# Performance work log

Hardware: AMD Instinct MI355X
Metric: run time of the kernel (lower is better)

## Reference

```python
import jax, jax.numpy as jnp
import numpy as np
import math
from jax import lax

WINDOWS = (3, 5, 7)
GRIDSIZE = 3
HALF_H = 384  # hidden of each directional LSTM (d_model // 2)


def _lstm_last(x, mask, Wih, Whh, bih, bhh, reverse):
    """Masked single-layer LSTM; returns final hidden state.
    x: [N, T, D], mask: [N, T] bool. Invalid steps leave (h, c) unchanged,
    which is equivalent to running the LSTM only over the valid contiguous
    sub-window (leading/trailing pads are skipped).
    PyTorch gate order: i, f, g, o.
    """
    N = x.shape[0]
    H = Whh.shape[1]
    h0 = jnp.zeros((N, H), x.dtype)
    c0 = jnp.zeros((N, H), x.dtype)

    def step(carry, inp):
        h, c = carry
        xt, mt = inp
        gates = xt @ Wih.T + h @ Whh.T + (bih + bhh)
        i, f, g, o = jnp.split(gates, 4, axis=-1)
        i = jax.nn.sigmoid(i); f = jax.nn.sigmoid(f); o = jax.nn.sigmoid(o)
        g = jnp.tanh(g)
        c_new = f * c + i * g
        h_new = o * jnp.tanh(c_new)
        m = mt[:, None]
        return (jnp.where(m, h_new, h), jnp.where(m, c_new, c)), None

    xs = (jnp.moveaxis(x, 1, 0), jnp.moveaxis(mask, 1, 0))
    (h, _), _ = lax.scan(step, (h0, c0), xs, reverse=reverse)
    return h


def setup_inputs() -> dict:
    key = jax.random.key(0)
    ks = jax.random.split(key, 12)
    B, L, D = 16, 512, 768
    H4 = 4 * HALF_H
    s = 0.02
    inp = {
        'sequence_output': jax.random.normal(ks[0], (B, L, D), jnp.float32),
        'Wih_f': jax.random.normal(ks[1], (3, H4, D), jnp.float32) * s,
        'Whh_f': jax.random.normal(ks[2], (3, H4, HALF_H), jnp.float32) * s,
        'bih_f': jax.random.normal(ks[3], (3, H4), jnp.float32) * s,
        'bhh_f': jax.random.normal(ks[4], (3, H4), jnp.float32) * s,
        'Wih_b': jax.random.normal(ks[5], (3, H4, D), jnp.float32) * s,
        'Whh_b': jax.random.normal(ks[6], (3, H4, HALF_H), jnp.float32) * s,
        'bih_b': jax.random.normal(ks[7], (3, H4), jnp.float32) * s,
        'bhh_b': jax.random.normal(ks[8], (3, H4), jnp.float32) * s,
        'kan_coeffs': jax.random.normal(ks[9], (2, 11, GRIDSIZE, D), jnp.float32)
                      / (np.sqrt(D) * np.sqrt(GRIDSIZE)),
        'kan_bias': jax.random.normal(ks[10], (11,), jnp.float32) * s,
        'valid_ids': jax.random.randint(ks[11], (B, L), 0, 2, jnp.int64),
    }
    return inp


def reference(sequence_output, Wih_f, Whh_f, bih_f, bhh_f,
              Wih_b, Whh_b, bih_b, bhh_b, kan_coeffs, kan_bias, valid_ids):
    B, L, D = sequence_output.shape
    # ---- valid-id compaction (scatter valid tokens to the front, zeros after)
    v = valid_ids == 1
    dest = jnp.where(v, jnp.cumsum(v, axis=1) - 1, L)  # invalid -> dump slot L
    bidx = jnp.arange(B)[:, None]
    valid_output = (jnp.zeros((B, L + 1, D), sequence_output.dtype)
                    .at[bidx, dest].set(sequence_output))[:, :L]
    x = valid_output  # dropout is identity in eval

    # ---- per-window sliding BiLSTM (vectorized over all B*L positions)
    outs = []
    for wi, w in enumerate(WINDOWS):
        half = w // 2
        idx = jnp.arange(L)[:, None] + jnp.arange(-half, half + 1)[None, :]  # [L,w]
        valid = (idx >= 0) & (idx < L)
        idxc = jnp.clip(idx, 0, L - 1)
        xw = x[:, idxc].reshape(B * L, w, D)                  # [B*L, w, D]
        m = jnp.broadcast_to(valid[None], (B, L, w)).reshape(B * L, w)
        hf = _lstm_last(xw, m, Wih_f[wi], Whh_f[wi], bih_f[wi], bhh_f[wi], False)
        hb = _lstm_last(xw, m, Wih_b[wi], Whh_b[wi], bih_b[wi], bhh_b[wi], True)
        outs.append(jnp.concatenate([hf, hb], axis=-1).reshape(B, L, D))

    seq = outs[0] + outs[1] + outs[2]

    # ---- 'dot-att' fusion over window features
    stk = jnp.stack(outs, axis=2)                             # [B, L, K, D]
    q = seq[:, :, None, :]                                    # [B, L, 1, D]
    attn = jax.nn.softmax(
        jnp.einsum('blqd,blkd->blqk', q, stk) / math.sqrt(D), axis=-1)
    local = jnp.einsum('blqk,blkd->blqd', attn, stk)[:, :, 0]
    seq = seq + local

    # ---- NaiveFourierKAN classifier (gridsize=3)
    k = jnp.arange(1, GRIDSIZE + 1, dtype=seq.dtype)
    xg = seq[..., None, :] * k[:, None]                       # [B, L, g, D]
    logits = (jnp.einsum('blgi,ogi->blo', jnp.cos(xg), kan_coeffs[0])
              + jnp.einsum('blgi,ogi->blo', jnp.sin(xg), kan_coeffs[1])
              + kan_bias)
    return logits
```

## Files before the change

kernel.cpp:

```cpp
#include <hip/hip_runtime.h>

#define BT 8192
#define SEQL 512
#define DIM 768
#define HID 384
#define NG 1536

using US = unsigned short;
typedef __bf16 bf16x8 __attribute__((ext_vector_type(8)));
typedef float f32x4 __attribute__((ext_vector_type(4)));

__device__ __forceinline__ float b2f(US u) {
  union { unsigned u; float f; } x; x.u = ((unsigned)u) << 16; return x.f;
}
__device__ __forceinline__ US f2b(float f) {
  __bf16 h = (__bf16)f;
  union { __bf16 h; US u; } x; x.h = h; return x.u;
}
__device__ __forceinline__ float fsig(float x) { return 1.f / (1.f + __expf(-x)); }
__device__ __forceinline__ float ftanh(float x) { return 1.f - 2.f / (__expf(2.f * x) + 1.f); }

__device__ __forceinline__ void gload16(const void* g, void* l) {
  __builtin_amdgcn_global_load_lds((const __attribute__((address_space(1))) unsigned*)g,
                                   (__attribute__((address_space(3))) unsigned*)l, 16, 0, 0);
}

__device__ __forceinline__ bf16x8 lds_frag(const US* base, int row, int colb, int swz) {
  return *(const bf16x8*)((const char*)base + row * 128 + (colb ^ swz));
}

__global__ __launch_bounds__(256) void convW_ih_k(const float* __restrict__ WihF,
                                                  const float* __restrict__ WihB,
                                                  US* __restrict__ WihP) {
  int d = blockIdx.z;
  const float* src = d ? WihB : WihF;
  size_t idx = (size_t)blockIdx.x * 256 + threadIdx.x;
  int lane = (int)(idx & 63);
  int t = (int)(idx >> 6);
  int sg = t & 3;
  int wn = (t >> 2) & 1;
  int kk = (t >> 3) & 1;
  int kt = (t >> 4) % 12;
  int nb = (t / 192) % 12;
  int wi = t / (192 * 12);
  int srow = sg * HID + nb * 32 + wn * 16 + (lane & 15);
  int scol = kt * 64 + kk * 32 + (lane >> 4) * 8;
  const float* s = src + ((size_t)wi * NG + srow) * DIM + scol;
  float4 v0 = *(const float4*)s;
  float4 v1 = *(const float4*)(s + 4);
  ushort4 o0, o1;
  o0.x = f2b(v0.x); o0.y = f2b(v0.y); o0.z = f2b(v0.z); o0.w = f2b(v0.w);
  o1.x = f2b(v1.x); o1.y = f2b(v1.y); o1.z = f2b(v1.z); o1.w = f2b(v1.w);
  US* dst = WihP + ((size_t)d * 442368 + idx) * 8;
  *(ushort4*)dst = o0;
  *(ushort4*)(dst + 4) = o1;
}

__global__ __launch_bounds__(256) void convW_hh_k(const float* __restrict__ WhhF,
                                                  const float* __restrict__ WhhB,
                                                  US* __restrict__ WhhP) {
  int d = blockIdx.z;
  const float* src = d ? WhhB : WhhF;
  size_t idx = (size_t)blockIdx.x * 256 + threadIdx.x;
  int lane = (int)(idx & 63);
  int t = (int)(idx >> 6);
  int sg = t & 3;
  int wn = (t >> 2) & 1;
  int kk = (t >> 3) & 1;
  int kt = (t >> 4) % 6;
  int hb = (t / 96) % 12;
  int wi = t / (96 * 12);
  int srow = sg * HID + hb * 32 + wn * 16 + (lane & 15);
  int scol = kt * 64 + kk * 32 + (lane >> 4) * 8;
  const float* s = src + ((size_t)wi * NG + srow) * HID + scol;
  float4 v0 = *(const float4*)s;
  float4 v1 = *(const float4*)(s + 4);
  ushort4 o0, o1;
  o0.x = f2b(v0.x); o0.y = f2b(v0.y); o0.z = f2b(v0.z); o0.w = f2b(v0.w);
  o1.x = f2b(v1.x); o1.y = f2b(v1.y); o1.z = f2b(v1.z); o1.w = f2b(v1.w);
  US* dst = WhhP + ((size_t)d * 221184 + idx) * 8;
  *(ushort4*)dst = o0;
  *(ushort4*)(dst + 4) = o1;
}

__global__ __launch_bounds__(256) void conv_coef_k(const float* __restrict__ coef,
                                                   US* __restrict__ coefP) {
  int idx = blockIdx.x * 256 + threadIdx.x;
  int s = idx & 31;
  int i = (idx >> 5) % DIM;
  int g = idx / (32 * DIM);
  float v = 0.f;
  int o = s & 15;
  if (o < 11) v = coef[(size_t)((s >> 4) * 33 + o * 3 + g) * DIM + i];
  coefP[idx] = f2b(v);
}

__global__ void scan_k(const int* __restrict__ valid, int* __restrict__ dest) {
  __shared__ int s[SEQL];
  int b = blockIdx.x, l = threadIdx.x;
  int v = (valid[b * SEQL + l] == 1) ? 1 : 0;
  s[l] = v;
  __syncthreads();
  for (int off = 1; off < SEQL; off <<= 1) {
    int t = (l >= off) ? s[l - off] : 0;
    __syncthreads();
    s[l] += t;
    __syncthreads();
  }
  dest[b * SEQL + l] = v ? (s[l] - 1) : -1;
}

__global__ __launch_bounds__(256) void scatter_k(const float* __restrict__ seq,
                                                 const int* __restrict__ dest,
                                                 US* __restrict__ xc) {
  int idx = blockIdx.x * 256 + threadIdx.x;
  int p = idx / 192, c = idx - p * 192;
  int d = dest[p];
  if (d < 0) return;
  int b = p >> 9;
  float4 v = ((const float4*)seq)[(size_t)p * 192 + c];
  ushort4 o;
  o.x = f2b(v.x); o.y = f2b(v.y); o.z = f2b(v.z); o.w = f2b(v.w);
  ((ushort4*)xc)[(size_t)(b * SEQL + d) * 192 + c] = o;
}

__global__ __launch_bounds__(256, 4) void gate_gemm_k(
    const US* __restrict__ xc, const US* __restrict__ WihP,
    const float* __restrict__ bihF, const float* __restrict__ bihB,
    const float* __restrict__ bhhF, const float* __restrict__ bhhB,
    US* __restrict__ G, int dirBase) {
  int zi = blockIdx.z;
  int wi = zi % 3, dr = dirBase + zi / 3;
  const float* bih = dr ? bihB : bihF;
  const float* bhh = dr ? bhhB : bhhF;
  int m0 = blockIdx.x * 128, nb = blockIdx.y;
  const US* Wp = WihP + ((size_t)(dr * 3 + wi) * 12 + nb) * (128 * DIM);
  US* Gw = G + (size_t)wi * BT * NG;
  __shared__ alignas(16) US As[2][128 * 64];
  __shared__ float biasS[128];
  int tid = threadIdx.x, lane = tid & 63, wid = tid >> 6;
  int wm = wid >> 1, wn = wid & 1;
  if (tid < 128) {
    int sg = tid >> 5, hl = tid & 31;
    int gc = wi * NG + sg * HID + nb * 32 + hl;
    biasS[tid] = bih[gc] + bhh[gc];
  }
  int r_in = lane >> 3;
  int cb = (lane & 7) * 16;
  int cb_src = cb ^ (r_in << 4);
  int swz = (lane & 7) << 4;
  f32x4 acc[4][4] = {};

  auto stageA = [&](US* dst, int k0) {
#pragma unroll
    for (int c = 0; c < 4; ++c) {
      int chk = wid * 4 + c;
      int row = chk * 8 + r_in;
      gload16((const char*)xc + ((size_t)(m0 + row) * DIM + k0) * 2 + cb_src,
              (char*)dst + chk * 1024);
    }
  };

  const US* Bbase = Wp + (size_t)wn * 4 * 512 + (size_t)lane * 8;

  stageA(As[0], 0);
  __syncthreads();
  int cur = 0;
  for (int kt = 0; kt < 12; ++kt) {
    int k0 = kt * 64;
    if (k0 + 64 < DIM) stageA(As[cur ^ 1], k0 + 64);
#pragma unroll
    for (int kk = 0; kk < 2; ++kk) {
      int colb = kk * 64 + (lane >> 4) * 16;
      bf16x8 a[4], b[4];
#pragma unroll
      for (int i = 0; i < 4; ++i)
        a[i] = lds_frag(As[cur], wm * 64 + i * 16 + (lane & 15), colb, swz);
      const US* bp = Bbase + (size_t)(kt * 2 + kk) * (2 * 4 * 512);
#pragma unroll
      for (int sg = 0; sg < 4; ++sg)
        b[sg] = *(const bf16x8*)(bp + (size_t)sg * 512);
#pragma unroll
      for (int mi = 0; mi < 4; ++mi)
#pragma unroll
        for (int sg = 0; sg < 4; ++sg)
          acc[mi][sg] = __builtin_amdgcn_mfma_f32_16x16x32_bf16(a[mi], b[sg], acc[mi][sg], 0, 0, 0);
    }
    __syncthreads();
    cur ^= 1;
  }
  int hh = wn * 16 + (lane & 15);
  int hidx = nb * 32 + hh;
#pragma unroll
  for (int mi = 0; mi < 4; ++mi) {
#pragma unroll
    for (int r = 0; r < 4; ++r) {
      int p = m0 + wm * 64 + mi * 16 + ((lane >> 4) << 2) + r;
      ushort4 gv;
      gv.x = f2b(acc[mi][0][r] + biasS[hh]);
      gv.y = f2b(acc[mi][1][r] + biasS[32 + hh]);
      gv.z = f2b(acc[mi][2][r] + biasS[64 + hh]);
      gv.w = f2b(acc[mi][3][r] + biasS[96 + hh]);
      *(ushort4*)&Gw[(size_t)p * NG + (size_t)hidx * 4] = gv;
    }
  }
}

__global__ __launch_bounds__(384) void step0_k(const US* __restrict__ G, US* __restrict__ C,
                                               US* __restrict__ hn, int dirBase) {
  int zi = blockIdx.z;
  int wi = zi % 3, dr = dirBase + zi / 3;
  int half = wi + 1;
  int dlt = dr ? half : -half;
  int p = blockIdx.x, hidx = threadIdx.x;
  int l = p & (SEQL - 1);
  const US* Gw = G + (size_t)wi * BT * NG;
  float c = 0.f, h = 0.f;
  int t = l + dlt;
  if ((unsigned)t < (unsigned)SEQL) {
    ushort4 gv = *(const ushort4*)&Gw[(size_t)(p + dlt) * NG + (size_t)hidx * 4];
    c = fsig(b2f(gv.x)) * ftanh(b2f(gv.z));
    h = fsig(b2f(gv.w)) * ftanh(c);
  }
  size_t o = (size_t)wi * BT * HID + (size_t)p * HID + hidx;
  C[o] = f2b(c);
  hn[o] = f2b(h);
}

__global__ __launch_bounds__(256, 4) void step_k(
    const US* __restrict__ WhhP,
    const US* __restrict__ G, US* __restrict__ C,
    const US* __restrict__ hcur, US* __restrict__ hnxt, US* __restrict__ Outs,
    int s, int wi0, int nact, int dirBase) {
  int zi = blockIdx.z;
  int wi = wi0 + zi % nact, dr = dirBase + zi / nact;
  int w = 2 * wi + 3, half = wi + 1;
  int j = dr ? (w - 1 - s) : s;
  int dlt = j - half;
  bool fin = (s == w - 1);
  const US* Gw = G + (size_t)wi * BT * NG;
  US* Cw = C + (size_t)wi * BT * HID;
  const US* hc = hcur + (size_t)wi * BT * HID;
  US* hn = hnxt + (size_t)wi * BT * HID;
  US* Ow = Outs + (size_t)wi * BT * DIM + (dr ? HID : 0);
  int m0 = blockIdx.x * 128, hb = blockIdx.y;
  const US* Wp = WhhP + ((size_t)(dr * 3 + wi) * 12 + hb) * (128 * HID);
  __shared__ alignas(16) US As[2][128 * 64];
  int tid = threadIdx.x, lane = tid & 63, wid = tid >> 6;
  int wm = wid >> 1, wn = wid & 1;
  int r_in = lane >> 3, cb = (lane & 7) * 16;
  int cb_src = cb ^ (r_in << 4);
  int swz = (lane & 7) << 4;
  f32x4 acc[4][4] = {};

  auto stageA = [&](US* dst, int k0) {
#pragma unroll
    for (int c = 0; c < 4; ++c) {
      int chk = wid * 4 + c;
      int row = chk * 8 + r_in;
      gload16((const char*)hc + ((size_t)(m0 + row) * HID + k0) * 2 + cb_src,
              (char*)dst + chk * 1024);
    }
  };

  const US* Bbase = Wp + (size_t)wn * 4 * 512 + (size_t)lane * 8;

  stageA(As[0], 0);
  __syncthreads();
  int cur = 0;
  for (int kt = 0; kt < 6; ++kt) {
    int k0 = kt * 64;
    if (k0 + 64 < HID) stageA(As[cur ^ 1], k0 + 64);
#pragma unroll
    for (int kk = 0; kk < 2; ++kk) {
      int colb = kk * 64 + (lane >> 4) * 16;
      bf16x8 a[4], b[4];
#pragma unroll
      for (int i = 0; i < 4; ++i)
        a[i] = lds_frag(As[cur], wm * 64 + i * 16 + (lane & 15), colb, swz);
      const US* bp = Bbase + (size_t)(kt * 2 + kk) * (2 * 4 * 512);
#pragma unroll
      for (int sg = 0; sg < 4; ++sg)
        b[sg] = *(const bf16x8*)(bp + (size_t)sg * 512);
#pragma unroll
      for (int mi = 0; mi < 4; ++mi)
#pragma unroll
        for (int sg = 0; sg < 4; ++sg)
          acc[mi][sg] = __builtin_amdgcn_mfma_f32_16x16x32_bf16(a[mi], b[sg], acc[mi][sg], 0, 0, 0);
    }
    __syncthreads();
    cur ^= 1;
  }
  int hh = wn * 16 + (lane & 15);
  int hidx = hb * 32 + hh;
#pragma unroll
  for (int mi = 0; mi < 4; ++mi) {
#pragma unroll
    for (int r = 0; r < 4; ++r) {
      int p = m0 + wm * 64 + mi * 16 + ((lane >> 4) << 2) + r;
      int l = p & (SEQL - 1);
      float hval;
      if ((unsigned)(l + dlt) < (unsigned)SEQL) {
        ushort4 gv = *(const ushort4*)&Gw[(size_t)(p + dlt) * NG + (size_t)hidx * 4];
        float gi = acc[mi][0][r] + b2f(gv.x);
        float gf = acc[mi][1][r] + b2f(gv.y);
        float gg = acc[mi][2][r] + b2f(gv.z);
        float go = acc[mi][3][r] + b2f(gv.w);
        size_t ci = (size_t)p * HID + hidx;
        float c = fsig(gf) * b2f(Cw[ci]) + fsig(gi) * ftanh(gg);
        Cw[ci] = f2b(c);
        hval = fsig(go) * ftanh(c);
      } else {
        hval = b2f(hc[(size_t)p * HID + hidx]);
      }
      if (fin) Ow[(size_t)p * DIM + hidx] = f2b(hval);
      else hn[(size_t)p * HID + hidx] = f2b(hval);
    }
  }
}

__global__ __launch_bounds__(256) void attn_kan_k(
    const US* __restrict__ Outs, const US* __restrict__ coefP,
    const float* __restrict__ kbias, float* __restrict__ out) {
  int p4 = blockIdx.x * 4;
  int tid = threadIdx.x, lane = tid & 63, wid = tid >> 6;
  __shared__ float red[176];
  float sq[3][4];
  {
    float o0[3][4], o1[3][4], o2[3][4], q[3][4];
#pragma unroll
    for (int c = 0; c < 3; ++c) {
      int i = tid + 256 * c;
#pragma unroll
      for (int t = 0; t < 4; ++t) {
        o0[c][t] = b2f(Outs[(size_t)(p4 + t) * DIM + i]);
        o1[c][t] = b2f(Outs[(size_t)(BT + p4 + t) * DIM + i]);
        o2[c][t] = b2f(Outs[(size_t)(2 * BT + p4 + t) * DIM + i]);
        q[c][t] = o0[c][t] + o1[c][t] + o2[c][t];
      }
    }
    float d[3][4];
#pragma unroll
    for (int t = 0; t < 4; ++t) {
      d[0][t] = 0.f; d[1][t] = 0.f; d[2][t] = 0.f;
#pragma unroll
      for (int c = 0; c < 3; ++c) {
        d[0][t] += q[c][t] * o0[c][t];
        d[1][t] += q[c][t] * o1[c][t];
        d[2][t] += q[c][t] * o2[c][t];
      }
    }
#pragma unroll
    for (int off = 32; off; off >>= 1)
#pragma unroll
      for (int t = 0; t < 4; ++t) {
        d[0][t] += __shfl_down(d[0][t], off);
        d[1][t] += __shfl_down(d[1][t], off);
        d[2][t] += __shfl_down(d[2][t], off);
      }
    if (lane == 0)
#pragma unroll
      for (int t = 0; t < 4; ++t) {
        red[(t * 3 + 0) * 4 + wid] = d[0][t];
        red[(t * 3 + 1) * 4 + wid] = d[1][t];
        red[(t * 3 + 2) * 4 + wid] = d[2][t];
      }
    __syncthreads();
    const float scl = 0.03608439182435161f;
#pragma unroll
    for (int t = 0; t < 4; ++t) {
      float s0 = (red[(t * 3) * 4] + red[(t * 3) * 4 + 1] + red[(t * 3) * 4 + 2] + red[(t * 3) * 4 + 3]) * scl;
      float s1 = (red[(t * 3 + 1) * 4] + red[(t * 3 + 1) * 4 + 1] + red[(t * 3 + 1) * 4 + 2] + red[(t * 3 + 1) * 4 + 3]) * scl;
      float s2 = (red[(t * 3 + 2) * 4] + red[(t * 3 + 2) * 4 + 1] + red[(t * 3 + 2) * 4 + 2] + red[(t * 3 + 2) * 4 + 3]) * scl;
      float mx = fmaxf(s0, fmaxf(s1, s2));
      float a0 = __expf(s0 - mx), a1 = __expf(s1 - mx), a2 = __expf(s2 - mx);
      float inv = 1.f / (a0 + a1 + a2);
      a0 *= inv; a1 *= inv; a2 *= inv;
#pragma unroll
      for (int c = 0; c < 3; ++c)
        sq[c][t] = q[c][t] + a0 * o0[c][t] + a1 * o1[c][t] + a2 * o2[c][t];
    }
  }
  float acc[11][4];
#pragma unroll
  for (int o = 0; o < 11; ++o)
#pragma unroll
    for (int t = 0; t < 4; ++t) acc[o][t] = 0.f;
#pragma unroll
  for (int c = 0; c < 3; ++c) {
    int i = tid + 256 * c;
#pragma unroll
    for (int g = 0; g < 3; ++g) {
      float sn[4], cs[4];
#pragma unroll
      for (int t = 0; t < 4; ++t) __sincosf(sq[c][t] * (float)(g + 1), &sn[t], &cs[t]);
      const US* cp = coefP + ((size_t)g * DIM + i) * 32;
      bf16x8 k0 = *(const bf16x8*)(cp);
      bf16x8 k1 = *(const bf16x8*)(cp + 8);
      bf16x8 k2 = *(const bf16x8*)(cp + 16);
      bf16x8 k3 = *(const bf16x8*)(cp + 24);
#pragma unroll
      for (int o = 0; o < 8; ++o) {
        float cc = (float)k0[o], ss = (float)k2[o];
#pragma unroll
        for (int t = 0; t < 4; ++t) acc[o][t] += cs[t] * cc + sn[t] * ss;
      }
#pragma unroll
      for (int o = 8; o < 11; ++o) {
        float cc = (float)k1[o - 8], ss = (float)k3[o - 8];
#pragma unroll
        for (int t = 0; t < 4; ++t) acc[o][t] += cs[t] * cc + sn[t] * ss;
      }
    }
  }
  __syncthreads();
#pragma unroll
  for (int o = 0; o < 11; ++o)
#pragma unroll
    for (int t = 0; t < 4; ++t) {
      float v = acc[o][t];
#pragma unroll
      for (int off = 32; off; off >>= 1) v += __shfl_down(v, off);
      if (lane == 0) red[(o * 4 + t) * 4 + wid] = v;
    }
  __syncthreads();
  if (tid < 44) {
    int o = tid >> 2, t = tid & 3;
    out[(size_t)(p4 + t) * 11 + o] =
        red[tid * 4] + red[tid * 4 + 1] + red[tid * 4 + 2] + red[tid * 4 + 3] + kbias[o];
  }
}

extern "C" void kernel_launch(void* const* d_in, const int* in_sizes, int n_in,
                              void* d_out, int out_size, void* d_ws, size_t ws_size,
                              hipStream_t stream) {
  const float* seq = (const float*)d_in[0];
  const float* WihF = (const float*)d_in[1];
  const float* WhhF = (const float*)d_in[2];
  const float* bihF = (const float*)d_in[3];
  const float* bhhF = (const float*)d_in[4];
  const float* WihB = (const float*)d_in[5];
  const float* WhhB = (const float*)d_in[6];
  const float* bihB = (const float*)d_in[7];
  const float* bhhB = (const float*)d_in[8];
  const float* coef = (const float*)d_in[9];
  const float* kbias = (const float*)d_in[10];
  const int* valid = (const int*)d_in[11];

  constexpr size_t SZ_XC = (size_t)BT * DIM * 2;
  constexpr size_t SZ_DEST = (size_t)BT * 4;
  constexpr size_t SZ_CP = (size_t)3 * DIM * 32 * 2;
  constexpr size_t SZ_G = (size_t)3 * BT * NG * 2;
  constexpr size_t SZ_C = (size_t)3 * BT * HID * 2;
  constexpr size_t SZ_H = (size_t)3 * BT * HID * 2;
  constexpr size_t SZ_OUTS = (size_t)3 * BT * DIM * 2;
  constexpr size_t SZ_WIHP = (size_t)2 * 3 * NG * DIM * 2;
  constexpr size_t SZ_WHHP = (size_t)2 * 3 * NG * HID * 2;
  constexpr size_t NEED = SZ_XC + SZ_DEST + SZ_CP + SZ_WIHP + SZ_WHHP +
                          SZ_G + SZ_C + 2 * SZ_H + SZ_OUTS;
  if (ws_size < NEED) return;

  char* ws = (char*)d_ws;
  US* xc = (US*)ws;                          ws += SZ_XC;
  int* dest = (int*)ws;                      ws += SZ_DEST;
  US* coefP = (US*)ws;                       ws += SZ_CP;
  US* WihP = (US*)ws;                        ws += SZ_WIHP;
  US* WhhP = (US*)ws;                        ws += SZ_WHHP;
  US* G = (US*)ws;                           ws += SZ_G;
  US* C = (US*)ws;                           ws += SZ_C;
  US* h0 = (US*)ws;                          ws += SZ_H;
  US* h1 = (US*)ws;                          ws += SZ_H;
  US* Outs = (US*)ws;
  float* out = (float*)d_out;

  hipMemsetAsync(xc, 0, SZ_XC, stream);
  scan_k<<<16, SEQL, 0, stream>>>(valid, dest);
  scatter_k<<<(BT * 192) / 256, 256, 0, stream>>>(seq, dest, xc);
  conv_coef_k<<<288, 256, 0, stream>>>(coef, coefP);
  convW_ih_k<<<dim3(442368 / 256, 1, 2), 256, 0, stream>>>(WihF, WihB, WihP);
  convW_hh_k<<<dim3(221184 / 256, 1, 2), 256, 0, stream>>>(WhhF, WhhB, WhhP);

  for (int dir = 0; dir < 2; ++dir) {
    gate_gemm_k<<<dim3(64, 12, 3), 256, 0, stream>>>(xc, WihP, bihF, bihB, bhhF, bhhB, G, dir);
    step0_k<<<dim3(BT, 1, 3), HID, 0, stream>>>(G, C, h1, dir);
    for (int s = 1; s < 7; ++s) {
      int nact = (s < 3) ? 3 : ((s < 5) ? 2 : 1);
      int wi0 = 3 - nact;
      US* hcur = (s & 1) ? h1 : h0;
      US* hnxt = (s & 1) ? h0 : h1;
      step_k<<<dim3(64, 12, nact), 256, 0, stream>>>(WhhP, G, C, hcur, hnxt, Outs,
                                                     s, wi0, nact, dir);
    }
  }
  attn_kan_k<<<BT / 4, 256, 0, stream>>>(Outs, coefP, kbias, out);
}
```

Baseline: 794.8 us.

## Fuse all LSTM recurrence steps into one persistent kernel with LDS-resident state

Replaces the per-timestep step0_k/step_k launches with a single kernel per direction. Each block owns 32 rows of one window and loops over all timesteps, keeping h and c in shared memory and never writing them to global memory. This removes about 14 launches and the global round trips of h and c. In exchange each block reloads the full Whh slice from global or L2 on every step, works on a small 32-row M tile with lower MFMA reuse, and has far fewer blocks per launch (768), so per-step weight bandwidth may become the bottleneck.

Measured after the change: 1.240 ms. 56.0% more time.

```diff
diff --git a/kernel.cpp b/kernel.cpp
--- a/kernel.cpp
+++ b/kernel.cpp
@@ -5,6 +5,7 @@
 #define DIM 768
 #define HID 384
 #define NG 1536
+#define FM 32
 
 using US = unsigned short;
 typedef __bf16 bf16x8 __attribute__((ext_vector_type(8)));
@@ -206,116 +207,88 @@
   }
 }
 
-__global__ __launch_bounds__(384) void step0_k(const US* __restrict__ G, US* __restrict__ C,
-                                               US* __restrict__ hn, int dirBase) {
-  int zi = blockIdx.z;
-  int wi = zi % 3, dr = dirBase + zi / 3;
-  int half = wi + 1;
-  int dlt = dr ? half : -half;
-  int p = blockIdx.x, hidx = threadIdx.x;
-  int l = p & (SEQL - 1);
+__global__ __launch_bounds__(256) void lstm_fused_k(
+    const US* __restrict__ WhhP, const US* __restrict__ G,
+    US* __restrict__ Outs, int dir) {
+  int x = blockIdx.x;
+  int wi = x % 3;
+  int m0 = (x / 3) * FM;
+  int w = 2 * wi + 3, half = wi + 1;
   const US* Gw = G + (size_t)wi * BT * NG;
-  float c = 0.f, h = 0.f;
-  int t = l + dlt;
-  if ((unsigned)t < (unsigned)SEQL) {
-    ushort4 gv = *(const ushort4*)&Gw[(size_t)(p + dlt) * NG + (size_t)hidx * 4];
-    c = fsig(b2f(gv.x)) * ftanh(b2f(gv.z));
-    h = fsig(b2f(gv.w)) * ftanh(c);
-  }
-  size_t o = (size_t)wi * BT * HID + (size_t)p * HID + hidx;
-  C[o] = f2b(c);
-  hn[o] = f2b(h);
-}
-
-__global__ __launch_bounds__(256, 4) void step_k(
-    const US* __restrict__ WhhP,
-    const US* __restrict__ G, US* __restrict__ C,
-    const US* __restrict__ hcur, US* __restrict__ hnxt, US* __restrict__ Outs,
-    int s, int wi0, int nact, int dirBase) {
-  int zi = blockIdx.z;
-  int wi = wi0 + zi % nact, dr = dirBase + zi / nact;
-  int w = 2 * wi + 3, half = wi + 1;
-  int j = dr ? (w - 1 - s) : s;
-  int dlt = j - half;
-  bool fin = (s == w - 1);
-  const US* Gw = G + (size_t)wi * BT * NG;
-  US* Cw = C + (size_t)wi * BT * HID;
-  const US* hc = hcur + (size_t)wi * BT * HID;
-  US* hn = hnxt + (size_t)wi * BT * HID;
-  US* Ow = Outs + (size_t)wi * BT * DIM + (dr ? HID : 0);
-  int m0 = blockIdx.x * 128, hb = blockIdx.y;
-  const US* Wp = WhhP + ((size_t)(dr * 3 + wi) * 12 + hb) * (128 * HID);
-  __shared__ alignas(16) US As[2][128 * 64];
-  int tid = threadIdx.x, lane = tid & 63, wid = tid >> 6;
-  int wm = wid >> 1, wn = wid & 1;
-  int r_in = lane >> 3, cb = (lane & 7) * 16;
-  int cb_src = cb ^ (r_in << 4);
-  int swz = (lane & 7) << 4;
-  f32x4 acc[4][4] = {};
-
-  auto stageA = [&](US* dst, int k0) {
-#pragma unroll
-    for (int c = 0; c < 4; ++c) {
-      int chk = wid * 4 + c;
-      int row = chk * 8 + r_in;
-      gload16((const char*)hc + ((size_t)(m0 + row) * HID + k0) * 2 + cb_src,
-              (char*)dst + chk * 1024);
-    }
-  };
-
-  const US* Bbase = Wp + (size_t)wn * 4 * 512 + (size_t)lane * 8;
-
-  stageA(As[0], 0);
-  __syncthreads();
-  int cur = 0;
-  for (int kt = 0; kt < 6; ++kt) {
-    int k0 = kt * 64;
-    if (k0 + 64 < HID) stageA(As[cur ^ 1], k0 + 64);
-#pragma unroll
-    for (int kk = 0; kk < 2; ++kk) {
-      int colb = kk * 64 + (lane >> 4) * 16;
-      bf16x8 a[4], b[4];
-#pragma unroll
-      for (int i = 0; i < 4; ++i)
-        a[i] = lds_frag(As[cur], wm * 64 + i * 16 + (lane & 15), colb, swz);
-      const US* bp = Bbase + (size_t)(kt * 2 + kk) * (2 * 4 * 512);
-#pragma unroll
-      for (int sg = 0; sg < 4; ++sg)
-        b[sg] = *(const bf16x8*)(bp + (size_t)sg * 512);
-#pragma unroll
-      for (int mi = 0; mi < 4; ++mi)
-#pragma unroll
-        for (int sg = 0; sg < 4; ++sg)
-          acc[mi][sg] = __builtin_amdgcn_mfma_f32_16x16x32_bf16(a[mi], b[sg], acc[mi][sg], 0, 0, 0);
+  US* Ow = Outs + (size_t)wi * BT * DIM + (dir ? HID : 0);
+  const US* WpB = WhhP + (size_t)(dir * 3 + wi) * 12 * (128 * HID);
+
+  __shared__ alignas(16) US h_lds[2][FM * HID];
+  __shared__ alignas(16) US c_lds[FM * HID];
+
+  int tid = threadIdx.x, lane = tid & 63, wv = tid >> 6;
+  int l15 = lane & 15, l4 = lane >> 4;
+
+  for (int s = 0; s < w; ++s) {
+    int j = dir ? (w - 1 - s) : s;
+    int dlt = j - half;
+    bool fin = (s == w - 1);
+    const US* hprev = h_lds[(s + 1) & 1];
+    US* hnext = h_lds[s & 1];
+
+#pragma unroll 1
+    for (int ch = 0; ch < 6; ++ch) {
+      int hbase = wv * 96 + ch * 16;
+      int hidx = hbase + l15;
+      f32x4 acc[2][4] = {};
+      if (s > 0) {
+        int hb = hbase >> 5, wn = (hbase >> 4) & 1;
+        const US* Bb = WpB + (size_t)hb * (128 * HID) + (size_t)wn * 2048 + (size_t)lane * 8;
+#pragma unroll
+        for (int kk = 0; kk < 12; ++kk) {
+          int colb = kk * 64 + l4 * 16;
+          bf16x8 a[2], b[4];
+#pragma unroll
+          for (int mi = 0; mi < 2; ++mi) {
+            int rr = mi * 16 + l15;
+            a[mi] = *(const bf16x8*)((const char*)hprev + rr * (HID * 2) +
+                                     (colb ^ ((rr & 7) << 4)));
+          }
+          const US* bp = Bb + (size_t)kk * 4096;
+#pragma unroll
+          for (int sg = 0; sg < 4; ++sg)
+            b[sg] = *(const bf16x8*)(bp + (size_t)sg * 512);
+#pragma unroll
+          for (int mi = 0; mi < 2; ++mi)
+#pragma unroll
+            for (int sg = 0; sg < 4; ++sg)
+              acc[mi][sg] = __builtin_amdgcn_mfma_f32_16x16x32_bf16(a[mi], b[sg], acc[mi][sg], 0, 0, 0);
+        }
+      }
+#pragma unroll
+      for (int mi = 0; mi < 2; ++mi) {
+#pragma unroll
+        for (int r = 0; r < 4; ++r) {
+          int rloc = mi * 16 + (l4 << 2) + r;
+          int p = m0 + rloc;
+          int l = p & (SEQL - 1);
+          int sb = rloc * (HID * 2) + ((hidx * 2) ^ ((rloc & 7) << 4));
+          float hval;
+          if ((unsigned)(l + dlt) < (unsigned)SEQL) {
+            ushort4 gv = *(const ushort4*)&Gw[(size_t)(p + dlt) * NG + (size_t)hidx * 4];
+            float gi = acc[mi][0][r] + b2f(gv.x);
+            float gf = acc[mi][1][r] + b2f(gv.y);
+            float gg = acc[mi][2][r] + b2f(gv.z);
+            float go = acc[mi][3][r] + b2f(gv.w);
+            float cold = (s == 0) ? 0.f : b2f(*(const US*)((const char*)c_lds + sb));
+            float c = fsig(gf) * cold + fsig(gi) * ftanh(gg);
+            *(US*)((char*)c_lds + sb) = f2b(c);
+            hval = fsig(go) * ftanh(c);
+          } else {
+            hval = (s == 0) ? 0.f : b2f(*(const US*)((const char*)hprev + sb));
+            if (s == 0) *(US*)((char*)c_lds + sb) = 0;
+          }
+          if (fin) Ow[(size_t)p * DIM + hidx] = f2b(hval);
+          else *(US*)((char*)hnext + sb) = f2b(hval);
+        }
+      }
     }
     __syncthreads();
-    cur ^= 1;
-  }
-  int hh = wn * 16 + (lane & 15);
-  int hidx = hb * 32 + hh;
-#pragma unroll
-  for (int mi = 0; mi < 4; ++mi) {
-#pragma unroll
-    for (int r = 0; r < 4; ++r) {
-      int p = m0 + wm * 64 + mi * 16 + ((lane >> 4) << 2) + r;
-      int l = p & (SEQL - 1);
-      float hval;
-      if ((unsigned)(l + dlt) < (unsigned)SEQL) {
-        ushort4 gv = *(const ushort4*)&Gw[(size_t)(p + dlt) * NG + (size_t)hidx * 4];
-        float gi = acc[mi][0][r] + b2f(gv.x);
-        float gf = acc[mi][1][r] + b2f(gv.y);
-        float gg = acc[mi][2][r] + b2f(gv.z);
-        float go = acc[mi][3][r] + b2f(gv.w);
-        size_t ci = (size_t)p * HID + hidx;
-        float c = fsig(gf) * b2f(Cw[ci]) + fsig(gi) * ftanh(gg);
-        Cw[ci] = f2b(c);
-        hval = fsig(go) * ftanh(c);
-      } else {
-        hval = b2f(hc[(size_t)p * HID + hidx]);
-      }
-      if (fin) Ow[(size_t)p * DIM + hidx] = f2b(hval);
-      else hn[(size_t)p * HID + hidx] = f2b(hval);
-    }
   }
 }
 
@@ -451,13 +424,11 @@
   constexpr size_t SZ_DEST = (size_t)BT * 4;
   constexpr size_t SZ_CP = (size_t)3 * DIM * 32 * 2;
   constexpr size_t SZ_G = (size_t)3 * BT * NG * 2;
-  constexpr size_t SZ_C = (size_t)3 * BT * HID * 2;
-  constexpr size_t SZ_H = (size_t)3 * BT * HID * 2;
   constexpr size_t SZ_OUTS = (size_t)3 * BT * DIM * 2;
   constexpr size_t SZ_WIHP = (size_t)2 * 3 * NG * DIM * 2;
   constexpr size_t SZ_WHHP = (size_t)2 * 3 * NG * HID * 2;
   constexpr size_t NEED = SZ_XC + SZ_DEST + SZ_CP + SZ_WIHP + SZ_WHHP +
-                          SZ_G + SZ_C + 2 * SZ_H + SZ_OUTS;
+                          SZ_G + SZ_OUTS;
   if (ws_size < NEED) return;
 
   char* ws = (char*)d_ws;
@@ -467,9 +438,6 @@
   US* WihP = (US*)ws;                        ws += SZ_WIHP;
   US* WhhP = (US*)ws;                        ws += SZ_WHHP;
   US* G = (US*)ws;                           ws += SZ_G;
-  US* C = (US*)ws;                           ws += SZ_C;
-  US* h0 = (US*)ws;                          ws += SZ_H;
-  US* h1 = (US*)ws;                          ws += SZ_H;
   US* Outs = (US*)ws;
   float* out = (float*)d_out;
 
@@ -482,15 +450,7 @@
 
   for (int dir = 0; dir < 2; ++dir) {
     gate_gemm_k<<<dim3(64, 12, 3), 256, 0, stream>>>(xc, WihP, bihF, bihB, bhhF, bhhB, G, dir);
-    step0_k<<<dim3(BT, 1, 3), HID, 0, stream>>>(G, C, h1, dir);
-    for (int s = 1; s < 7; ++s) {
-      int nact = (s < 3) ? 3 : ((s < 5) ? 2 : 1);
-      int wi0 = 3 - nact;
-      US* hcur = (s & 1) ? h1 : h0;
-      US* hnxt = (s & 1) ? h0 : h1;
-      step_k<<<dim3(64, 12, nact), 256, 0, stream>>>(WhhP, G, C, hcur, hnxt, Outs,
-                                                     s, wi0, nact, dir);
-    }
+    lstm_fused_k<<<(BT / FM) * 3, 256, 0, stream>>>(WhhP, G, Outs, dir);
   }
   attn_kan_k<<<BT / 4, 256, 0, stream>>>(Outs, coefP, kbias, out);
 }
```

## Pre-pack activations into MFMA fragment layout and drop LDS staging in GEMMs

Applied to the files above, without the earlier changes.

The compacted input xc and the hidden-state buffers are now written directly in a fragment-packed panel layout (pk_off), matching the layout already used for the weights. The gate GEMM and recurrent step GEMM then load A fragments straight from global memory with coalesced 16-byte loads, removing the global_load_lds staging, LDS swizzle reads, double buffering and the per-iteration barriers. This trades LDS reuse and software pipelining for simpler direct loads that depend on L1/L2 caching. Scatter, step0 and the step epilogue write hidden state in the packed layout.

Result: no change. 805.6 us (+1.4%).

```diff
diff --git a/kernel.cpp b/kernel.cpp
--- a/kernel.cpp
+++ b/kernel.cpp
@@ -20,13 +20,10 @@
 __device__ __forceinline__ float fsig(float x) { return 1.f / (1.f + __expf(-x)); }
 __device__ __forceinline__ float ftanh(float x) { return 1.f - 2.f / (__expf(2.f * x) + 1.f); }
 
-__device__ __forceinline__ void gload16(const void* g, void* l) {
-  __builtin_amdgcn_global_load_lds((const __attribute__((address_space(1))) unsigned*)g,
-                                   (__attribute__((address_space(3))) unsigned*)l, 16, 0, 0);
-}
-
-__device__ __forceinline__ bf16x8 lds_frag(const US* base, int row, int colb, int swz) {
-  return *(const bf16x8*)((const char*)base + row * 128 + (colb ^ swz));
+__device__ __forceinline__ size_t pk_off(int panel, int rloc, int col, int panelStride) {
+  return (size_t)panel * panelStride + (col >> 6) * 8192 + ((col >> 5) & 1) * 4096 +
+         (rloc >> 6) * 2048 + ((rloc >> 4) & 3) * 512 +
+         (((rloc & 15) | (((col & 31) >> 3) << 4))) * 8 + (col & 7);
 }
 
 __global__ __launch_bounds__(256) void convW_ih_k(const float* __restrict__ WihF,
@@ -112,20 +109,23 @@
 
 __global__ __launch_bounds__(256) void scatter_k(const float* __restrict__ seq,
                                                  const int* __restrict__ dest,
-                                                 US* __restrict__ xc) {
+                                                 US* __restrict__ xcP) {
   int idx = blockIdx.x * 256 + threadIdx.x;
-  int p = idx / 192, c = idx - p * 192;
+  int p = idx / 192, cc = idx - p * 192;
   int d = dest[p];
   if (d < 0) return;
   int b = p >> 9;
-  float4 v = ((const float4*)seq)[(size_t)p * 192 + c];
+  float4 v = ((const float4*)seq)[(size_t)p * 192 + cc];
   ushort4 o;
   o.x = f2b(v.x); o.y = f2b(v.y); o.z = f2b(v.z); o.w = f2b(v.w);
-  ((ushort4*)xc)[(size_t)(b * SEQL + d) * 192 + c] = o;
+  int pdst = b * SEQL + d;
+  int c = cc * 4;
+  size_t off = pk_off(pdst >> 7, pdst & 127, c, 98304);
+  *(ushort4*)&xcP[off] = o;
 }
 
 __global__ __launch_bounds__(256, 4) void gate_gemm_k(
-    const US* __restrict__ xc, const US* __restrict__ WihP,
+    const US* __restrict__ xcP, const US* __restrict__ WihP,
     const float* __restrict__ bihF, const float* __restrict__ bihB,
     const float* __restrict__ bhhF, const float* __restrict__ bhhB,
     US* __restrict__ G, int dirBase) {
@@ -133,10 +133,9 @@
   int wi = zi % 3, dr = dirBase + zi / 3;
   const float* bih = dr ? bihB : bihF;
   const float* bhh = dr ? bhhB : bhhF;
-  int m0 = blockIdx.x * 128, nb = blockIdx.y;
-  const US* Wp = WihP + ((size_t)(dr * 3 + wi) * 12 + nb) * (128 * DIM);
+  int panel = blockIdx.x, nb = blockIdx.y;
+  const US* Wp = WihP + ((size_t)(dr * 3 + wi) * 12 + nb) * 98304;
   US* Gw = G + (size_t)wi * BT * NG;
-  __shared__ alignas(16) US As[2][128 * 64];
   __shared__ float biasS[128];
   int tid = threadIdx.x, lane = tid & 63, wid = tid >> 6;
   int wm = wid >> 1, wn = wid & 1;
@@ -145,52 +144,28 @@
     int gc = wi * NG + sg * HID + nb * 32 + hl;
     biasS[tid] = bih[gc] + bhh[gc];
   }
-  int r_in = lane >> 3;
-  int cb = (lane & 7) * 16;
-  int cb_src = cb ^ (r_in << 4);
-  int swz = (lane & 7) << 4;
+  __syncthreads();
   f32x4 acc[4][4] = {};
-
-  auto stageA = [&](US* dst, int k0) {
-#pragma unroll
-    for (int c = 0; c < 4; ++c) {
-      int chk = wid * 4 + c;
-      int row = chk * 8 + r_in;
-      gload16((const char*)xc + ((size_t)(m0 + row) * DIM + k0) * 2 + cb_src,
-              (char*)dst + chk * 1024);
-    }
-  };
-
-  const US* Bbase = Wp + (size_t)wn * 4 * 512 + (size_t)lane * 8;
-
-  stageA(As[0], 0);
-  __syncthreads();
-  int cur = 0;
-  for (int kt = 0; kt < 12; ++kt) {
-    int k0 = kt * 64;
-    if (k0 + 64 < DIM) stageA(As[cur ^ 1], k0 + 64);
-#pragma unroll
-    for (int kk = 0; kk < 2; ++kk) {
-      int colb = kk * 64 + (lane >> 4) * 16;
-      bf16x8 a[4], b[4];
-#pragma unroll
-      for (int i = 0; i < 4; ++i)
-        a[i] = lds_frag(As[cur], wm * 64 + i * 16 + (lane & 15), colb, swz);
-      const US* bp = Bbase + (size_t)(kt * 2 + kk) * (2 * 4 * 512);
+  const US* Ab = xcP + (size_t)panel * 98304 + (size_t)wm * 2048 + (size_t)lane * 8;
+  const US* Bb = Wp + (size_t)wn * 2048 + (size_t)lane * 8;
+#pragma unroll 2
+  for (int kp = 0; kp < 24; ++kp) {
+    bf16x8 a[4], b[4];
+    const US* ap = Ab + (size_t)kp * 4096;
+    const US* bp = Bb + (size_t)kp * 4096;
+#pragma unroll
+    for (int mi = 0; mi < 4; ++mi) a[mi] = *(const bf16x8*)(ap + (size_t)mi * 512);
+#pragma unroll
+    for (int sg = 0; sg < 4; ++sg) b[sg] = *(const bf16x8*)(bp + (size_t)sg * 512);
+#pragma unroll
+    for (int mi = 0; mi < 4; ++mi)
 #pragma unroll
       for (int sg = 0; sg < 4; ++sg)
-        b[sg] = *(const bf16x8*)(bp + (size_t)sg * 512);
-#pragma unroll
-      for (int mi = 0; mi < 4; ++mi)
-#pragma unroll
-        for (int sg = 0; sg < 4; ++sg)
-          acc[mi][sg] = __builtin_amdgcn_mfma_f32_16x16x32_bf16(a[mi], b[sg], acc[mi][sg], 0, 0, 0);
-    }
-    __syncthreads();
-    cur ^= 1;
+        acc[mi][sg] = __builtin_amdgcn_mfma_f32_16x16x32_bf16(a[mi], b[sg], acc[mi][sg], 0, 0, 0);
   }
   int hh = wn * 16 + (lane & 15);
   int hidx = nb * 32 + hh;
+  int m0 = panel * 128;
 #pragma unroll
   for (int mi = 0; mi < 4; ++mi) {
 #pragma unroll
@@ -222,9 +197,8 @@
     c = fsig(b2f(gv.x)) * ftanh(b2f(gv.z));
     h = fsig(b2f(gv.w)) * ftanh(c);
   }
-  size_t o = (size_t)wi * BT * HID + (size_t)p * HID + hidx;
-  C[o] = f2b(c);
-  hn[o] = f2b(h);
+  C[(size_t)wi * BT * HID + (size_t)p * HID + hidx] = f2b(c);
+  hn[(size_t)wi * BT * HID + pk_off(p >> 7, p & 127, hidx, 49152)] = f2b(h);
 }
 
 __global__ __launch_bounds__(256, 4) void step_k(
@@ -243,62 +217,42 @@
   const US* hc = hcur + (size_t)wi * BT * HID;
   US* hn = hnxt + (size_t)wi * BT * HID;
   US* Ow = Outs + (size_t)wi * BT * DIM + (dr ? HID : 0);
-  int m0 = blockIdx.x * 128, hb = blockIdx.y;
-  const US* Wp = WhhP + ((size_t)(dr * 3 + wi) * 12 + hb) * (128 * HID);
-  __shared__ alignas(16) US As[2][128 * 64];
+  int panel = blockIdx.x, hb = blockIdx.y;
+  const US* Wp = WhhP + ((size_t)(dr * 3 + wi) * 12 + hb) * 49152;
   int tid = threadIdx.x, lane = tid & 63, wid = tid >> 6;
   int wm = wid >> 1, wn = wid & 1;
-  int r_in = lane >> 3, cb = (lane & 7) * 16;
-  int cb_src = cb ^ (r_in << 4);
-  int swz = (lane & 7) << 4;
   f32x4 acc[4][4] = {};
 
-  auto stageA = [&](US* dst, int k0) {
-#pragma unroll
-    for (int c = 0; c < 4; ++c) {
-      int chk = wid * 4 + c;
-      int row = chk * 8 + r_in;
-      gload16((const char*)hc + ((size_t)(m0 + row) * HID + k0) * 2 + cb_src,
-              (char*)dst + chk * 1024);
-    }
-  };
-
-  const US* Bbase = Wp + (size_t)wn * 4 * 512 + (size_t)lane * 8;
-
-  stageA(As[0], 0);
-  __syncthreads();
-  int cur = 0;
-  for (int kt = 0; kt < 6; ++kt) {
-    int k0 = kt * 64;
-    if (k0 + 64 < HID) stageA(As[cur ^ 1], k0 + 64);
-#pragma unroll
-    for (int kk = 0; kk < 2; ++kk) {
-      int colb = kk * 64 + (lane >> 4) * 16;
-      bf16x8 a[4], b[4];
-#pragma unroll
-      for (int i = 0; i < 4; ++i)
-        a[i] = lds_frag(As[cur], wm * 64 + i * 16 + (lane & 15), colb, swz);
-      const US* bp = Bbase + (size_t)(kt * 2 + kk) * (2 * 4 * 512);
+  const US* Ab = hc + (size_t)panel * 49152 + (size_t)wm * 2048 + (size_t)lane * 8;
+  const US* Bb = Wp + (size_t)wn * 2048 + (size_t)lane * 8;
+#pragma unroll 2
+  for (int kp = 0; kp < 12; ++kp) {
+    bf16x8 a[4], b[4];
+    const US* ap = Ab + (size_t)kp * 4096;
+    const US* bp = Bb + (size_t)kp * 4096;
+#pragma unroll
+    for (int mi = 0; mi < 4; ++mi) a[mi] = *(const bf16x8*)(ap + (size_t)mi * 512);
+#pragma unroll
+    for (int sg = 0; sg < 4; ++sg) b[sg] = *(const bf16x8*)(bp + (size_t)sg * 512);
+#pragma unroll
+    for (int mi = 0; mi < 4; ++mi)
 #pragma unroll
       for (int sg = 0; sg < 4; ++sg)
-        b[sg] = *(const bf16x8*)(bp + (size_t)sg * 512);
-#pragma unroll
-      for (int mi = 0; mi < 4; ++mi)
-#pragma unroll
-        for (int sg = 0; sg < 4; ++sg)
-          acc[mi][sg] = __builtin_amdgcn_mfma_f32_16x16x32_bf16(a[mi], b[sg], acc[mi][sg], 0, 0, 0);
-    }
-    __syncthreads();
-    cur ^= 1;
-  }
-  int hh = wn * 16 + (lane & 15);
+        acc[mi][sg] = __builtin_amdgcn_mfma_f32_16x16x32_bf16(a[mi], b[sg], acc[mi][sg], 0, 0, 0);
+  }
+  int l15 = lane & 15, l4 = lane >> 4;
+  int hh = wn * 16 + l15;
   int hidx = hb * 32 + hh;
+  int m0 = panel * 128;
+  size_t wbase = (size_t)panel * 49152 + (size_t)hb * 4096 + (size_t)wm * 2048 +
+                 (size_t)(wn * 2 + (l15 >> 3)) * 128 + (l15 & 7);
 #pragma unroll
   for (int mi = 0; mi < 4; ++mi) {
 #pragma unroll
     for (int r = 0; r < 4; ++r) {
-      int p = m0 + wm * 64 + mi * 16 + ((lane >> 4) << 2) + r;
+      int p = m0 + wm * 64 + mi * 16 + (l4 << 2) + r;
       int l = p & (SEQL - 1);
+      size_t po = wbase + (size_t)mi * 512 + (size_t)((l4 << 2) + r) * 8;
       float hval;
       if ((unsigned)(l + dlt) < (unsigned)SEQL) {
         ushort4 gv = *(const ushort4*)&Gw[(size_t)(p + dlt) * NG + (size_t)hidx * 4];
@@ -311,10 +265,10 @@
         Cw[ci] = f2b(c);
         hval = fsig(go) * ftanh(c);
       } else {
-        hval = b2f(hc[(size_t)p * HID + hidx]);
+        hval = b2f(hc[po]);
       }
       if (fin) Ow[(size_t)p * DIM + hidx] = f2b(hval);
-      else hn[(size_t)p * HID + hidx] = f2b(hval);
+      else hn[po] = f2b(hval);
     }
   }
 }
@@ -461,7 +415,7 @@
   if (ws_size < NEED) return;
 
   char* ws = (char*)d_ws;
-  US* xc = (US*)ws;                          ws += SZ_XC;
+  US* xcP = (US*)ws;                         ws += SZ_XC;
   int* dest = (int*)ws;                      ws += SZ_DEST;
   US* coefP = (US*)ws;                       ws += SZ_CP;
   US* WihP = (US*)ws;                        ws += SZ_WIHP;
@@ -473,15 +427,15 @@
   US* Outs = (US*)ws;
   float* out = (float*)d_out;
 
-  hipMemsetAsync(xc, 0, SZ_XC, stream);
+  hipMemsetAsync(xcP, 0, SZ_XC, stream);
   scan_k<<<16, SEQL, 0, stream>>>(valid, dest);
-  scatter_k<<<(BT * 192) / 256, 256, 0, stream>>>(seq, dest, xc);
+  scatter_k<<<(BT * 192) / 256, 256, 0, stream>>>(seq, dest, xcP);
   conv_coef_k<<<288, 256, 0, stream>>>(coef, coefP);
   convW_ih_k<<<dim3(442368 / 256, 1, 2), 256, 0, stream>>>(WihF, WihB, WihP);
   convW_hh_k<<<dim3(221184 / 256, 1, 2), 256, 0, stream>>>(WhhF, WhhB, WhhP);
 
   for (int dir = 0; dir < 2; ++dir) {
-    gate_gemm_k<<<dim3(64, 12, 3), 256, 0, stream>>>(xc, WihP, bihF, bihB, bhhF, bhhB, G, dir);
+    gate_gemm_k<<<dim3(64, 12, 3), 256, 0, stream>>>(xcP, WihP, bihF, bihB, bhhF, bhhB, G, dir);
     step0_k<<<dim3(BT, 1, 3), HID, 0, stream>>>(G, C, h1, dir);
     for (int s = 1; s < 7; ++s) {
       int nact = (s < 3) ? 3 : ((s < 5) ? 2 : 1);
```
